# Performance work log

Measured on AMD Instinct MI355X. Metric: run time of the kernel, lower is better.

## Reference

```python
import jax, jax.numpy as jnp
import numpy as np

N = 50000      # nodes
E = 600000     # edges
G = 8          # graphs in the batch (for mean_nodes)
D = 128        # input_dim == hidden_dim
OUT = 10       # out_dim
NEG_SLOPE = 0.01  # nn.LeakyReLU default


def _lin(k, fi, fo):
    return jax.random.normal(k, (fi, fo), jnp.float32) / np.sqrt(fi).astype(np.float32)


def setup_inputs() -> dict:
    key = jax.random.key(0)
    ks = jax.random.split(key, 12)
    inputs = jax.random.normal(ks[0], (N, D), jnp.float32)
    src = jax.random.randint(ks[1], (E,), 0, N)
    dst = jax.random.randint(ks[2], (E,), 0, N)
    graph_id = jnp.sort(jax.random.randint(ks[3], (N,), 0, G))
    return {
        "inputs": inputs,
        "src": src,
        "dst": dst,
        "graph_id": graph_id,
        # GraphConv weights (DGL GraphConv: y = norm * A_norm x W + b)
        "W1": _lin(ks[4], D, D), "b1": jnp.zeros((D,), jnp.float32),
        "W2": _lin(ks[5], D, D), "b2": jnp.zeros((D,), jnp.float32),
        "W3": _lin(ks[6], D, D), "b3": jnp.zeros((D,), jnp.float32),
        # classifier head
        "Wc1": _lin(ks[7], D, 512),  "bc1": jnp.zeros((512,), jnp.float32),
        "Wc2": _lin(ks[8], 512, 256), "bc2": jnp.zeros((256,), jnp.float32),
        "Wc3": _lin(ks[9], 256, OUT), "bc3": jnp.zeros((OUT,), jnp.float32),
    }


def reference(inputs, src, dst, graph_id, W1, b1, W2, b2, W3, b3,
              Wc1, bc1, Wc2, bc2, Wc3, bc3):
    # DGL GraphConv with norm='both': h = D_in^{-1/2} A D_out^{-1/2} x W + b
    ones_e = jnp.ones((E,), jnp.float32)
    out_deg = jax.ops.segment_sum(ones_e, src, num_segments=N)
    in_deg = jax.ops.segment_sum(ones_e, dst, num_segments=N)
    src_norm = jnp.clip(out_deg, 1.0, None) ** -0.5   # [N]
    dst_norm = jnp.clip(in_deg, 1.0, None) ** -0.5    # [N]

    def gconv(x, W, b):
        x = x * src_norm[:, None]
        x = x @ W                                      # project first (in>=out)
        agg = jax.ops.segment_sum(x[src], dst, num_segments=N)  # SpMM
        return agg * dst_norm[:, None] + b

    h = gconv(inputs, W1, b1)
    h = gconv(h, W2, b2)
    h = gconv(h, W3, b3)

    # dgl.mean_nodes: per-graph mean over nodes
    sums = jax.ops.segment_sum(h, graph_id, num_segments=G)         # [G, D]
    cnts = jax.ops.segment_sum(jnp.ones((N,), jnp.float32), graph_id, num_segments=G)
    pooled = sums / jnp.clip(cnts, 1.0, None)[:, None]

    lrelu = lambda v: jax.nn.leaky_relu(v, NEG_SLOPE)
    x = lrelu(pooled @ Wc1 + bc1)
    x = lrelu(x @ Wc2 + bc2)
    x = lrelu(x @ Wc3 + bc3)
    return x
```

## Files before the change

### kernel.cpp

```cpp
#include <hip/hip_runtime.h>

#define Nn 50000
#define Ee 600000
#define Gg 8
#define Dd 128
#define NP 50048
#define NCHUNK 49

#define HWORDS 25024
#define HB 16
#define HIST_BLOCKS (2 * HB)
#define W12_BLOCKS 16
#define W123_BLOCKS 64
#define DTILE 64
#define DPBLK ((Nn + DTILE - 1) / DTILE)
#define RA_BLOCKS 128
#define RA_CHUNK ((DPBLK + RA_BLOCKS - 1) / RA_BLOCKS)

__global__ __launch_bounds__(1024) void hist_kernel(
    const int* __restrict__ src, const int* __restrict__ dst,
    unsigned int* __restrict__ phist,
    const float* __restrict__ W1, const float* __restrict__ W2,
    const float* __restrict__ W3, const float* __restrict__ b1,
    const float* __restrict__ b2,
    float* __restrict__ W12, float* __restrict__ e1, float* __restrict__ e2,
    int* __restrict__ accz)
{
    __shared__ unsigned int h[HWORDS];
    int t = threadIdx.x;
    int b = blockIdx.x;

    if (b < HIST_BLOCKS) {
        for (int i = t; i < HWORDS; i += 1024) h[i] = 0u;
        __syncthreads();
        int part = b >> 1;
        const int* arr = (b & 1) ? dst : src;
        int e0 = part * (Ee / HB);
        int eN = e0 + (Ee / HB);
        for (int e = e0 + t; e < eN; e += 1024) {
            int n = arr[e];
            atomicAdd(&h[n >> 1], 1u << ((n & 1) << 4));
        }
        __syncthreads();
        unsigned int* out = phist + (size_t)b * HWORDS;
        for (int i = t; i < HWORDS; i += 1024) out[i] = h[i];
    } else if (b < HIST_BLOCKS + W12_BLOCKS) {
        int j = (b - HIST_BLOCKS) * 8 + (t & 7);
        int k = t >> 3;
        float a = 0.f;
#pragma unroll 8
        for (int m = 0; m < 128; ++m) a += W1[k * 128 + m] * W2[m * 128 + j];
        W12[k * 128 + j] = a;
    } else {
        if (t < 128) {
            float a = 0.f;
#pragma unroll 8
            for (int k = 0; k < 128; ++k) a += b1[k] * W2[k * 128 + t];
            e1[t] = a;
        } else if (t < 256) {
            int c = t - 128;
            float a = 0.f;
#pragma unroll 8
            for (int k = 0; k < 128; ++k) a += b2[k] * W3[k * 128 + c];
            e2[c] = a;
        } else if (t < 256 + 88) {
            accz[t - 256] = 0;
        }
    }
}

__global__ __launch_bounds__(256) void scan_fused(
    const unsigned int* __restrict__ phist, const int* __restrict__ gid,
    float* __restrict__ srcn, float* __restrict__ pq, float* __restrict__ z,
    int* __restrict__ cnt, int* __restrict__ row_ptr, int* __restrict__ cursor,
    int* __restrict__ fs,
    const float* __restrict__ W12, const float* __restrict__ W3,
    const float* __restrict__ e1,
    float* __restrict__ W123, float* __restrict__ e1b)
{
    int b = blockIdx.x, t = threadIdx.x;
    if (b < NCHUNK) {
        __shared__ int tsum[256];
        __shared__ int lc[Gg];
        __shared__ int pre[64];
        __shared__ int sbase;
        if (t < Gg) lc[t] = 0;
        __syncthreads();

        int d4[4];
        int wbase = b * 512 + t * 2;
#pragma unroll
        for (int wi = 0; wi < 2; ++wi) {
            int w = wbase + wi;
            unsigned so0 = 0, so1 = 0, si0 = 0, si1 = 0;
            if (w < HWORDS) {
#pragma unroll
                for (int p = 0; p < HB; ++p) {
                    unsigned a  = phist[(size_t)(2 * p) * HWORDS + w];
                    unsigned bb = phist[(size_t)(2 * p + 1) * HWORDS + w];
                    so0 += a & 0xffffu; so1 += a >> 16;
                    si0 += bb & 0xffffu; si1 += bb >> 16;
                }
            }
#pragma unroll
            for (int hh = 0; hh < 2; ++hh) {
                int n = 2 * w + hh;
                unsigned so = hh ? so1 : so0, si = hh ? si1 : si0;
                int d = 0;
                if (n < Nn) {
                    d = (int)so;
                    float sn = 1.f / sqrtf(fmaxf((float)so, 1.f));
                    float dn = 1.f / sqrtf(fmaxf((float)si, 1.f));
                    srcn[n] = sn; pq[n] = sn * dn;
                    int g = gid[n];
                    atomicAdd(&lc[g], 1);
                    float zr[8];
#pragma unroll
                    for (int gg = 0; gg < 8; ++gg) zr[gg] = (gg == g) ? dn : 0.f;
                    *(float4*)(z + (size_t)n * 8)     = *(float4*)zr;
                    *(float4*)(z + (size_t)n * 8 + 4) = *(float4*)(zr + 4);
                }
                d4[wi * 2 + hh] = d;
            }
        }
        int s = (d4[0] + d4[1]) + (d4[2] + d4[3]);
        tsum[t] = s;
        __syncthreads();
        for (int off = 1; off < 256; off <<= 1) {
            int x = (t >= off) ? tsum[t - off] : 0;
            __syncthreads();
            tsum[t] += x;
            __syncthreads();
        }
        int run = tsum[t] - s;

        if (t == 0) atomicExch(&fs[b], (tsum[255] << 1) | 1);
        if (t < b) {
            int r;
            do { r = atomicAdd(&fs[t], 0); } while (!(r & 1));
            pre[t] = r >> 1;
        }
        __syncthreads();
        if (t == 0) {
            int base = 0;
            for (int p = 0; p < b; ++p) base += pre[p];
            sbase = base;
        }
        __syncthreads();

        int gpos = sbase + run;
#pragma unroll
        for (int i = 0; i < 4; ++i) {
            int n = b * 1024 + t * 4 + i;
            if (n < Nn) { row_ptr[n] = gpos; cursor[n] = gpos; }
            gpos += d4[i];
        }
        if (b == NCHUNK - 1 && t == 255) row_ptr[Nn] = Ee;
        __syncthreads();
        if (t < Gg && lc[t] > 0) atomicAdd(&cnt[t], lc[t]);
    } else if (b < NCHUNK + W123_BLOCKS) {
        int j = (b - NCHUNK) * 2 + (t & 1);
        int k = t >> 1;
        float a = 0.f;
#pragma unroll 8
        for (int m = 0; m < 128; ++m) a += W12[k * 128 + m] * W3[m * 128 + j];
        W123[k * 128 + j] = a;
    } else {
        if (t < 128) {
            float a = 0.f;
#pragma unroll 8
            for (int k = 0; k < 128; ++k) a += e1[k] * W3[k * 128 + t];
            e1b[t] = a;
        }
    }
}

__global__ __launch_bounds__(256) void fill_kernel(
    const int* __restrict__ src, const int* __restrict__ dst,
    int* __restrict__ cursor, int* __restrict__ csr_dst)
{
    int e0 = blockIdx.x * 512 + threadIdx.x;
    int e1 = e0 + 256;
    int s0 = -1, d0 = 0, s1 = -1, d1 = 0;
    if (e0 < Ee) { s0 = src[e0]; d0 = dst[e0]; }
    if (e1 < Ee) { s1 = src[e1]; d1 = dst[e1]; }
    if (s0 >= 0) { int p = atomicAdd(&cursor[s0], 1); csr_dst[p] = d0; }
    if (s1 >= 0) { int p = atomicAdd(&cursor[s1], 1); csr_dst[p] = d1; }
}

__global__ __launch_bounds__(256) void bspmm_kernel(
    const float* __restrict__ uin, const int* __restrict__ row_ptr,
    const int* __restrict__ csr, const float* __restrict__ pqv,
    float* __restrict__ uout, const float* __restrict__ sn,
    float* __restrict__ pwout)
{
    int t = threadIdx.x;
    int g = t & 7;
    int m = blockIdx.x * 32 + (t >> 3);
    float acc = 0.f, snm = 0.f;
    if (m < Nn) {
        int beg = row_ptr[m], end = row_ptr[m + 1];
        int j = beg;
        float a0 = 0.f, a1 = 0.f, a2 = 0.f, a3 = 0.f;
        float a4 = 0.f, a5 = 0.f, a6 = 0.f, a7 = 0.f;
        for (; j + 7 < end; j += 8) {
            int i0 = csr[j],     i1 = csr[j + 1], i2 = csr[j + 2], i3 = csr[j + 3];
            int i4 = csr[j + 4], i5 = csr[j + 5], i6 = csr[j + 6], i7 = csr[j + 7];
            a0 += uin[(size_t)i0 * 8 + g]; a1 += uin[(size_t)i1 * 8 + g];
            a2 += uin[(size_t)i2 * 8 + g]; a3 += uin[(size_t)i3 * 8 + g];
            a4 += uin[(size_t)i4 * 8 + g]; a5 += uin[(size_t)i5 * 8 + g];
            a6 += uin[(size_t)i6 * 8 + g]; a7 += uin[(size_t)i7 * 8 + g];
        }
        for (; j + 3 < end; j += 4) {
            int i0 = csr[j], i1 = csr[j + 1], i2 = csr[j + 2], i3 = csr[j + 3];
            a0 += uin[(size_t)i0 * 8 + g]; a1 += uin[(size_t)i1 * 8 + g];
            a2 += uin[(size_t)i2 * 8 + g]; a3 += uin[(size_t)i3 * 8 + g];
        }
        for (; j < end; ++j) a0 += uin[(size_t)csr[j] * 8 + g];
        acc = ((a0 + a1) + (a2 + a3)) + ((a4 + a5) + (a6 + a7));
        uout[(size_t)m * 8 + g] = pqv[m] * acc;
        if (pwout) snm = sn[m];
    }
    if (pwout) {
        __shared__ float red[Gg];
        if (t < Gg) red[t] = 0.f;
        __syncthreads();
        float v = snm * acc;
        v += __shfl_xor(v, 8, 64);
        v += __shfl_xor(v, 16, 64);
        v += __shfl_xor(v, 32, 64);
        if ((t & 63) < 8) atomicAdd(&red[t & 7], v);
        __syncthreads();
        if (t < Gg) atomicAdd(&pwout[t], red[t]);
    }
}

__global__ __launch_bounds__(256) void dotpool_kernel(
    const float* __restrict__ x, const float* __restrict__ u2p,
    const float* __restrict__ sn,
    const int* __restrict__ row_ptr, const int* __restrict__ csr,
    float* __restrict__ partial)
{
    __shared__ float xs[DTILE][Dd];
    __shared__ float f[DTILE][Gg];
    int t = threadIdx.x;
    int n0 = blockIdx.x * DTILE;

    {
        const float4* x4 = (const float4*)x;
        float4* xs4 = (float4*)xs;
#pragma unroll
        for (int k = 0; k < 8; ++k) {
            int idx = t + 256 * k;
            int i = idx >> 5;
            int n = n0 + i;
            xs4[idx] = (n < Nn) ? x4[(size_t)n * 32 + (idx & 31)]
                                : make_float4(0.f, 0.f, 0.f, 0.f);
        }
    }

    {
        int i = t >> 2, sub = t & 3;
        int n = n0 + i;
        float ax = 0.f, ay = 0.f, s = 0.f;
        if (n < Nn) {
            s = sn[n];
            int beg = row_ptr[n], end = row_ptr[n + 1];
            int j = beg;
            float bx = 0.f, by = 0.f, cx = 0.f, cy = 0.f, dx = 0.f, dy = 0.f;
            for (; j + 3 < end; j += 4) {
                int i0 = csr[j], i1 = csr[j + 1], i2 = csr[j + 2], i3 = csr[j + 3];
                float2 u0 = *(const float2*)(u2p + (size_t)i0 * 8 + sub * 2);
                float2 u1 = *(const float2*)(u2p + (size_t)i1 * 8 + sub * 2);
                float2 u2 = *(const float2*)(u2p + (size_t)i2 * 8 + sub * 2);
                float2 u3 = *(const float2*)(u2p + (size_t)i3 * 8 + sub * 2);
                ax += u0.x; ay += u0.y; bx += u1.x; by += u1.y;
                cx += u2.x; cy += u2.y; dx += u3.x; dy += u3.y;
            }
            for (; j < end; ++j) {
                float2 u = *(const float2*)(u2p + (size_t)csr[j] * 8 + sub * 2);
                ax += u.x; ay += u.y;
            }
            ax += bx + cx + dx; ay += by + cy + dy;
        }
        f[i][sub * 2 + 0] = s * ax;
        f[i][sub * 2 + 1] = s * ay;
    }
    __syncthreads();

    {
        int g = t >> 5, c = t & 31;
        float4 acc = {0.f, 0.f, 0.f, 0.f};
#pragma unroll 8
        for (int i = 0; i < DTILE; ++i) {
            float fv = f[i][g];
            float4 xv = *(const float4*)&xs[i][c * 4];
            acc.x += fv * xv.x; acc.y += fv * xv.y;
            acc.z += fv * xv.z; acc.w += fv * xv.w;
        }
        *(float4*)(partial + (size_t)blockIdx.x * 1024 + g * 128 + c * 4) = acc;
    }
}

__global__ __launch_bounds__(256) void dotreduceA_kernel(
    const float* __restrict__ partial, float* __restrict__ partial2)
{
    int b = blockIdx.x, t = threadIdx.x;
    int p0 = b * RA_CHUNK;
    int p1 = p0 + RA_CHUNK; if (p1 > DPBLK) p1 = DPBLK;
    float a0 = 0.f, a1 = 0.f, a2 = 0.f, a3 = 0.f;
    for (int p = p0; p < p1; ++p) {
        const float* pp = partial + (size_t)p * 1024;
        a0 += pp[t];
        a1 += pp[t + 256];
        a2 += pp[t + 512];
        a3 += pp[t + 768];
    }
    float* o = partial2 + (size_t)b * 1024;
    o[t] = a0; o[t + 256] = a1; o[t + 512] = a2; o[t + 768] = a3;
}

__global__ __launch_bounds__(256) void redfc1_kernel(
    const float* __restrict__ partial2, const float* __restrict__ pw1r,
    const float* __restrict__ pw2r, const int* __restrict__ cnt,
    const float* __restrict__ W123, const float* __restrict__ e1b,
    const float* __restrict__ e2, const float* __restrict__ b3,
    const float* __restrict__ Wc1, const float* __restrict__ bc1,
    float* __restrict__ x1g)
{
    __shared__ float prow[128];
    __shared__ float x0row[128];
    __shared__ float psum[256];
    int b = blockIdx.x, t = threadIdx.x;
    int g = b >> 2, q = b & 3;

    {
        int k = t & 127, h = t >> 7;
        float a0 = 0.f, a1 = 0.f;
        int p0 = h * 64;
        for (int p = p0; p < p0 + 64; p += 2) {
            a0 += partial2[(size_t)p * 1024 + g * 128 + k];
            a1 += partial2[(size_t)(p + 1) * 1024 + g * 128 + k];
        }
        psum[t] = a0 + a1;
        __syncthreads();
        if (t < 128) prow[t] = psum[t] + psum[t + 128];
        __syncthreads();
    }
    {
        int c = t & 127, h = t >> 7;
        float a = 0.f;
        int k0 = h * 64;
#pragma unroll 8
        for (int k = k0; k < k0 + 64; ++k) a += prow[k] * W123[k * 128 + c];
        psum[t] = a;
        __syncthreads();
        if (t < 128) {
            float inv = 1.f / fmaxf((float)cnt[g], 1.f);
            x0row[t] = (psum[t] + psum[t + 128]) * inv
                     + (pw2r[g] * inv) * e1b[t] + (pw1r[g] * inv) * e2[t] + b3[t];
        }
        __syncthreads();
    }
    {
        int m = q * 128 + (t & 127), h = t >> 7;
        float a = 0.f;
        int k0 = h * 64;
#pragma unroll 8
        for (int k = k0; k < k0 + 64; ++k)
            a += x0row[k] * Wc1[(size_t)k * 512 + m];
        psum[t] = a;
        __syncthreads();
        if (t < 128) {
            int m2 = q * 128 + t;
            float v = psum[t] + psum[t + 128] + bc1[m2];
            x1g[g * 512 + m2] = v > 0.f ? v : 0.01f * v;
        }
    }
}

__global__ __launch_bounds__(256) void fc2_kernel(
    const float* __restrict__ x1g, const float* __restrict__ Wc2,
    const float* __restrict__ bc2, float* __restrict__ x2g)
{
    __shared__ float xs[Gg * 512];
    __shared__ float par[256];
    int t = threadIdx.x;
    for (int i = t; i < Gg * 512; i += 256) xs[i] = x1g[i];
    __syncthreads();
    int q = t >> 6, rem = t & 63;
    int g = rem >> 3, m = blockIdx.x * 8 + (rem & 7);
    int k0 = q * 128;
    float a = 0.f;
#pragma unroll 16
    for (int k = 0; k < 128; ++k) a += xs[g * 512 + k0 + k] * Wc2[(size_t)(k0 + k) * 256 + m];
    par[t] = a;
    __syncthreads();
    if (t < 64) {
        float v = par[t] + par[t + 64] + par[t + 128] + par[t + 192] + bc2[m];
        x2g[g * 256 + m] = v > 0.f ? v : 0.01f * v;
    }
}

__global__ __launch_bounds__(640) void fc3_kernel(
    const float* __restrict__ x2g, const float* __restrict__ Wc3,
    const float* __restrict__ bc3, float* __restrict__ out)
{
    __shared__ float xs[Gg * 256];
    int t = threadIdx.x;
    for (int i = t; i < Gg * 256; i += 640) xs[i] = x2g[i];
    __syncthreads();
    int w = t >> 6, lane = t & 63;
    if (w < 10) {
        float acc[Gg];
#pragma unroll
        for (int g = 0; g < Gg; ++g) acc[g] = 0.f;
#pragma unroll
        for (int kk = 0; kk < 4; ++kk) {
            int k = lane + kk * 64;
            float wv = Wc3[(size_t)k * 10 + w];
#pragma unroll
            for (int g = 0; g < Gg; ++g) acc[g] += xs[g * 256 + k] * wv;
        }
#pragma unroll
        for (int g = 0; g < Gg; ++g) {
            float v = acc[g];
            for (int off = 32; off; off >>= 1) v += __shfl_down(v, off, 64);
            if (lane == 0) {
                v += bc3[w];
                out[g * 10 + w] = v > 0.f ? v : 0.01f * v;
            }
        }
    }
}

extern "C" void kernel_launch(void* const* d_in, const int* in_sizes, int n_in,
                              void* d_out, int out_size, void* d_ws, size_t ws_size,
                              hipStream_t stream)
{
    const float* inputs = (const float*)d_in[0];
    const int*   src    = (const int*)d_in[1];
    const int*   dst    = (const int*)d_in[2];
    const int*   gid    = (const int*)d_in[3];
    const float* W1  = (const float*)d_in[4];
    const float* b1  = (const float*)d_in[5];
    const float* W2  = (const float*)d_in[6];
    const float* b2  = (const float*)d_in[7];
    const float* W3  = (const float*)d_in[8];
    const float* b3  = (const float*)d_in[9];
    const float* Wc1 = (const float*)d_in[10];
    const float* bc1 = (const float*)d_in[11];
    const float* Wc2 = (const float*)d_in[12];
    const float* bc2 = (const float*)d_in[13];
    const float* Wc3 = (const float*)d_in[14];
    const float* bc3 = (const float*)d_in[15];

    int*   wi      = (int*)d_ws;
    int*   row_ptr = wi;
    int*   cursor  = row_ptr + NP;
    int*   csr_dst = cursor + NP;
    float* wf      = (float*)(csr_dst + Ee);
    float* srcn    = wf;
    float* pq      = srcn + NP;
    float* z       = pq + NP;
    float* u1      = z + (size_t)NP * 8;
    float* u2      = u1 + (size_t)NP * 8;
    float* partial = u2 + (size_t)NP * 8;
    float* partial2= partial + (size_t)DPBLK * 1024;
    float* pw1     = partial2 + (size_t)RA_BLOCKS * 1024;
    float* pw2     = pw1 + Gg;
    int*   cnt     = (int*)(pw2 + Gg);
    int*   fs      = cnt + Gg;
    float* W12v    = (float*)(fs + 64);
    float* W123v   = W12v + 128 * 128;
    float* e1v     = W123v + 128 * 128;
    float* e1bv    = e1v + 128;
    float* e2v     = e1bv + 128;
    float* x1g     = e2v + 128;
    float* x2g     = x1g + 4096;
    unsigned int* phist = (unsigned int*)(x2g + 2048);

    hist_kernel<<<HIST_BLOCKS + W12_BLOCKS + 1, 1024, 0, stream>>>(
        src, dst, phist, W1, W2, W3, b1, b2, W12v, e1v, e2v, (int*)pw1);
    scan_fused<<<NCHUNK + W123_BLOCKS + 1, 256, 0, stream>>>(
        phist, gid, srcn, pq, z, cnt, row_ptr, cursor, fs,
        W12v, W3, e1v, W123v, e1bv);
    fill_kernel<<<(Ee + 511) / 512, 256, 0, stream>>>(src, dst, cursor, csr_dst);

    int bblocks = (Nn + 31) / 32;
    bspmm_kernel<<<bblocks, 256, 0, stream>>>(z, row_ptr, csr_dst, pq,
                                              u1, srcn, pw1);
    bspmm_kernel<<<bblocks, 256, 0, stream>>>(u1, row_ptr, csr_dst, pq,
                                              u2, srcn, pw2);

    dotpool_kernel<<<DPBLK, 256, 0, stream>>>(inputs, u2, srcn,
                                              row_ptr, csr_dst, partial);
    dotreduceA_kernel<<<RA_BLOCKS, 256, 0, stream>>>(partial, partial2);
    redfc1_kernel<<<32, 256, 0, stream>>>(partial2, pw1, pw2, cnt,
                                          W123v, e1bv, e2v, b3, Wc1, bc1, x1g);
    fc2_kernel<<<32, 256, 0, stream>>>(x1g, Wc2, bc2, x2g);
    fc3_kernel<<<1, 640, 0, stream>>>(x2g, Wc3, bc3, (float*)d_out);
}
```

Baseline: 171.3 us.

## Fill CSR with per-block LDS cursors seeded from partial histograms

Replaces the global-atomic cursor array in the CSR fill with 16 blocks that each build a local cursor table in shared memory. The table is the prefix sum of earlier chunks' packed 16-bit partial histograms, so slot positions come from LDS atomics plus row_ptr. This drops the global cursor array, its initialisation in the scan kernel, and contended global atomics. The cost is only 16 blocks doing the fill, each spending time on a serial prefix over the partial histograms, which limits parallelism on a large GPU.

```diff
diff --git a/kernel.cpp b/kernel.cpp
--- a/kernel.cpp
+++ b/kernel.cpp
@@ -72,7 +72,7 @@
 __global__ __launch_bounds__(256) void scan_fused(
     const unsigned int* __restrict__ phist, const int* __restrict__ gid,
     float* __restrict__ srcn, float* __restrict__ pq, float* __restrict__ z,
-    int* __restrict__ cnt, int* __restrict__ row_ptr, int* __restrict__ cursor,
+    int* __restrict__ cnt, int* __restrict__ row_ptr,
     int* __restrict__ fs,
     const float* __restrict__ W12, const float* __restrict__ W3,
     const float* __restrict__ e1,
@@ -152,7 +152,7 @@
 #pragma unroll
         for (int i = 0; i < 4; ++i) {
             int n = b * 1024 + t * 4 + i;
-            if (n < Nn) { row_ptr[n] = gpos; cursor[n] = gpos; }
+            if (n < Nn) row_ptr[n] = gpos;
             gpos += d4[i];
         }
         if (b == NCHUNK - 1 && t == 255) row_ptr[Nn] = Ee;
@@ -175,17 +175,30 @@
     }
 }
 
-__global__ __launch_bounds__(256) void fill_kernel(
+__global__ __launch_bounds__(1024) void fill_kernel(
     const int* __restrict__ src, const int* __restrict__ dst,
-    int* __restrict__ cursor, int* __restrict__ csr_dst)
-{
-    int e0 = blockIdx.x * 512 + threadIdx.x;
-    int e1 = e0 + 256;
-    int s0 = -1, d0 = 0, s1 = -1, d1 = 0;
-    if (e0 < Ee) { s0 = src[e0]; d0 = dst[e0]; }
-    if (e1 < Ee) { s1 = src[e1]; d1 = dst[e1]; }
-    if (s0 >= 0) { int p = atomicAdd(&cursor[s0], 1); csr_dst[p] = d0; }
-    if (s1 >= 0) { int p = atomicAdd(&cursor[s1], 1); csr_dst[p] = d1; }
+    const int* __restrict__ row_ptr, const unsigned int* __restrict__ phist,
+    int* __restrict__ csr_dst)
+{
+    __shared__ unsigned int lcur[HWORDS];
+    int t = threadIdx.x, c = blockIdx.x;
+
+    for (int w = t; w < HWORDS; w += 1024) {
+        unsigned a = 0;
+        for (int p = 0; p < c; ++p) a += phist[(size_t)(2 * p) * HWORDS + w];
+        lcur[w] = a;
+    }
+    __syncthreads();
+
+    int e0 = c * (Ee / HB);
+    int e1 = e0 + (Ee / HB);
+    for (int e = e0 + t; e < e1; e += 1024) {
+        int s = src[e];
+        int sh = (s & 1) << 4;
+        unsigned old = atomicAdd(&lcur[s >> 1], 1u << sh);
+        int lr = (old >> sh) & 0xffff;
+        csr_dst[row_ptr[s] + lr] = dst[e];
+    }
 }
 
 __global__ __launch_bounds__(256) void bspmm_kernel(
@@ -457,8 +470,7 @@
 
     int*   wi      = (int*)d_ws;
     int*   row_ptr = wi;
-    int*   cursor  = row_ptr + NP;
-    int*   csr_dst = cursor + NP;
+    int*   csr_dst = row_ptr + NP;
     float* wf      = (float*)(csr_dst + Ee);
     float* srcn    = wf;
     float* pq      = srcn + NP;
@@ -483,9 +495,9 @@
     hist_kernel<<<HIST_BLOCKS + W12_BLOCKS + 1, 1024, 0, stream>>>(
         src, dst, phist, W1, W2, W3, b1, b2, W12v, e1v, e2v, (int*)pw1);
     scan_fused<<<NCHUNK + W123_BLOCKS + 1, 256, 0, stream>>>(
-        phist, gid, srcn, pq, z, cnt, row_ptr, cursor, fs,
+        phist, gid, srcn, pq, z, cnt, row_ptr, fs,
         W12v, W3, e1v, W123v, e1bv);
-    fill_kernel<<<(Ee + 511) / 512, 256, 0, stream>>>(src, dst, cursor, csr_dst);
+    fill_kernel<<<HB, 1024, 0, stream>>>(src, dst, row_ptr, phist, csr_dst);
 
     int bblocks = (Nn + 31) / 32;
     bspmm_kernel<<<bblocks, 256, 0, stream>>>(z, row_ptr, csr_dst, pq,
```

New measurement: 250.6 us. +46.3%, slower.
